# Kernel optimization log

Measured on AMD Instinct MI355X. Metric: run time of the kernel, lower is better.

## Reference

```python
import jax, jax.numpy as jnp
import numpy as np

D_MODEL = 1024
N_HEAD = 16
D_HEAD = D_MODEL // N_HEAD
N_EXPERTS = 8
TOP_K = 2
D_FF = 4096
EPS = 1e-6


def setup_inputs() -> dict:
    key = jax.random.key(0)
    ks = jax.random.split(key, 16)
    s = 0.02  # init scale
    d, dff, E = D_MODEL, D_FF, N_EXPERTS
    return {
        "dec": jax.random.normal(ks[0], (4, 1024, d), jnp.float32),
        "text_encoder": jax.random.normal(ks[1], (4, 512, d), jnp.float32),
        # self-attention projections
        "Wq1": jax.random.normal(ks[2], (d, d), jnp.float32) * s,
        "Wk1": jax.random.normal(ks[3], (d, d), jnp.float32) * s,
        "Wv1": jax.random.normal(ks[4], (d, d), jnp.float32) * s,
        "Wo1": jax.random.normal(ks[5], (d, d), jnp.float32) * s,
        # cross-attention projections
        "Wq2": jax.random.normal(ks[6], (d, d), jnp.float32) * s,
        "Wk2": jax.random.normal(ks[7], (d, d), jnp.float32) * s,
        "Wv2": jax.random.normal(ks[8], (d, d), jnp.float32) * s,
        "Wo2": jax.random.normal(ks[9], (d, d), jnp.float32) * s,
        # shared RMSNorm gain (module uses one norm instance three times)
        "g": jnp.ones((d,), jnp.float32),
        # MoE router + per-expert FFN weights
        "Wg": jax.random.normal(ks[10], (d, E), jnp.float32) * s,
        "W1": jax.random.normal(ks[11], (E, d, dff), jnp.float32) * s,
        "W2": jax.random.normal(ks[12], (E, dff, d), jnp.float32) * s,
    }


def rmsnorm(x, g):
    return x * jax.lax.rsqrt(jnp.mean(x * x, axis=-1, keepdims=True) + EPS) * g


def mha(q_in, k_in, v_in, Wq, Wk, Wv, Wo):
    B, Sq, _ = q_in.shape
    Sk = k_in.shape[1]
    q = (q_in @ Wq).reshape(B, Sq, N_HEAD, D_HEAD)
    k = (k_in @ Wk).reshape(B, Sk, N_HEAD, D_HEAD)
    v = (v_in @ Wv).reshape(B, Sk, N_HEAD, D_HEAD)
    scores = jnp.einsum("bqhd,bkhd->bhqk", q, k) / jnp.sqrt(jnp.asarray(D_HEAD, q.dtype))
    attn = jax.nn.softmax(scores, axis=-1)
    out = jnp.einsum("bhqk,bkhd->bqhd", attn, v).reshape(B, Sq, D_MODEL)
    return out @ Wo


def moe(x, Wg, W1, W2):
    # top-k softmax router, renormalized weights; dense per-expert FFN with combine
    probs = jax.nn.softmax(x @ Wg, axis=-1)              # [B,S,E]
    weights, indices = jax.lax.top_k(probs, TOP_K)        # [B,S,k]
    weights = weights / jnp.sum(weights, axis=-1, keepdims=True)
    # combine[t,e] = sum_k weights[t,k] * (indices[t,k]==e)
    combine = jnp.sum(
        jax.nn.one_hot(indices, N_EXPERTS, dtype=x.dtype) * weights[..., None], axis=-2
    )  # [B,S,E]
    out = jnp.zeros_like(x)
    for e in range(N_EXPERTS):  # fixed small expert loop
        h = jax.nn.relu(x @ W1[e]) @ W2[e]
        out = out + combine[..., e:e + 1] * h
    return weights, indices, out


def reference(dec, text_encoder, Wq1, Wk1, Wv1, Wo1, Wq2, Wk2, Wv2, Wo2, g, Wg, W1, W2):
    # self-attention + residual + RMSNorm (dropout p=0 -> identity)
    x = rmsnorm(mha(dec, dec, dec, Wq1, Wk1, Wv1, Wo1) + dec, g)
    # cross-attention + residual + RMSNorm
    x = rmsnorm(mha(x, text_encoder, text_encoder, Wq2, Wk2, Wv2, Wo2) + x, g)
    # MoE FFN + residual + RMSNorm
    weights, indices, y = moe(x, Wg, W1, W2)
    x = rmsnorm(y + x, g)
    return weights, indices, x
```

## Files before the change

### kernel.cpp

```cpp
#include <hip/hip_runtime.h>
#include <stdint.h>

#define D_    1024
#define BB    4
#define SDEC  1024
#define STXT  512
#define TDEC  4096
#define TTXT  2048
#define NH    16
#define DHD   64
#define NE    8
#define DFF   4096
#define NSLOT 8192
#define ND1   8192
#define ND2   4096
#define MOEGRID 512

using u16 = unsigned short;
typedef __attribute__((ext_vector_type(8))) short bf16x8;
typedef __attribute__((ext_vector_type(4))) float f32x4;

__device__ __forceinline__ float bf2f(u16 h) {
    union { unsigned int u; float f; } x; x.u = ((unsigned int)h) << 16; return x.f;
}
__device__ __forceinline__ u16 f2bf(float f) {
    union { float f; unsigned int u; } x; x.f = f;
    unsigned int lsb = (x.u >> 16) & 1u;
    return (u16)((x.u + 0x7fffu + lsb) >> 16);
}

__device__ __forceinline__ void gld16(const u16* g, u16* l) {
    __builtin_amdgcn_global_load_lds((const __attribute__((address_space(1))) void*)g,
                                     (__attribute__((address_space(3))) void*)l,
                                     16, 0, 0);
}

constexpr int BM = 128, BK = 32;

template<int SPLIT, int EPI, int BROWS>
__global__ __launch_bounds__(256) void gemm_bt(
    const u16* __restrict__ AH, const u16* __restrict__ AL,
    const u16* __restrict__ BH, const u16* __restrict__ BL,
    float* __restrict__ Cf, u16* __restrict__ CH, u16* __restrict__ CL,
    int M, int N, int K, int lda, int ldb, int ldc,
    long strA, long strB, long strC)
{
    constexpr int WM = (BROWS == 64) ? 2 : 4;
    constexpr int ASZ = BM * BK, BSZ = BROWS * BK;
    __shared__ u16 smem[(SPLIT ? 2 : 1) * (ASZ + BSZ)];
    u16* sAH = smem;
    u16* sBH = smem + ASZ;
    u16* sAL = SPLIT ? smem + ASZ + BSZ : nullptr;
    u16* sBL = SPLIT ? smem + 2 * ASZ + BSZ : nullptr;

    const int z = blockIdx.z;
    const long zA = (long)z * strA, zB = (long)z * strB, zC = (long)z * strC;

    const int tileM = blockIdx.y * BM, tileN = blockIdx.x * BROWS;
    const int t = threadIdx.x;
    const int sr = t >> 2;
    const int sc = (t & 3) << 3;
    const u16* pA = AH + zA + (long)(tileM + sr) * lda + sc;
    const u16* pB = BH + zB + (long)(tileN + sr) * ldb + sc;
    const u16* pAl = nullptr; const u16* pBl = nullptr;
    if constexpr (SPLIT) {
        pAl = AL + zA + (long)(tileM + sr) * lda + sc;
        pBl = BL + zB + (long)(tileN + sr) * ldb + sc;
    }
    const long hA = 64L * lda, hB = 64L * ldb;

    const int lane = t & 63;
    const int wv = t >> 6;
    const int wr = (BROWS == 64) ? (wv << 5) : ((wv >> 1) << 6);
    const int wc = (BROWS == 64) ? 0 : ((wv & 1) << 6);
    const int fr = lane & 15, kg = lane >> 4;

    f32x4 acc[WM][4];
    const f32x4 vzero = {0.f, 0.f, 0.f, 0.f};
#pragma unroll
    for (int m = 0; m < WM; ++m)
#pragma unroll
        for (int n = 0; n < 4; ++n) acc[m][n] = vzero;

    for (int k0 = 0; k0 < K; k0 += BK) {
        gld16(pA + k0,      sAH + t * 8);
        gld16(pA + k0 + hA, sAH + 2048 + t * 8);
        gld16(pB + k0,      sBH + t * 8);
        if constexpr (BROWS == 128) gld16(pB + k0 + hB, sBH + 2048 + t * 8);
        if constexpr (SPLIT) {
            gld16(pAl + k0,      sAL + t * 8);
            gld16(pAl + k0 + hA, sAL + 2048 + t * 8);
            gld16(pBl + k0,      sBL + t * 8);
            if constexpr (BROWS == 128) gld16(pBl + k0 + hB, sBL + 2048 + t * 8);
        }
        __syncthreads();

        bf16x8 fa[WM], fb[4], fal[WM], fbl[4];
#pragma unroll
        for (int m = 0; m < WM; ++m) {
            fa[m] = *(const bf16x8*)&sAH[(wr + m * 16 + fr) * BK + (kg << 3)];
            if constexpr (SPLIT) fal[m] = *(const bf16x8*)&sAL[(wr + m * 16 + fr) * BK + (kg << 3)];
        }
#pragma unroll
        for (int n = 0; n < 4; ++n) {
            fb[n] = *(const bf16x8*)&sBH[(wc + n * 16 + fr) * BK + (kg << 3)];
            if constexpr (SPLIT) fbl[n] = *(const bf16x8*)&sBL[(wc + n * 16 + fr) * BK + (kg << 3)];
        }
#pragma unroll
        for (int m = 0; m < WM; ++m)
#pragma unroll
            for (int n = 0; n < 4; ++n) {
                acc[m][n] = __builtin_amdgcn_mfma_f32_16x16x32_bf16(fa[m], fb[n], acc[m][n], 0, 0, 0);
                if constexpr (SPLIT) {
                    acc[m][n] = __builtin_amdgcn_mfma_f32_16x16x32_bf16(fa[m],  fbl[n], acc[m][n], 0, 0, 0);
                    acc[m][n] = __builtin_amdgcn_mfma_f32_16x16x32_bf16(fal[m], fb[n],  acc[m][n], 0, 0, 0);
                }
            }
        __syncthreads();
    }

#pragma unroll
    for (int m = 0; m < WM; ++m) {
        const int r0 = tileM + wr + m * 16 + (kg << 2);
#pragma unroll
        for (int n = 0; n < 4; ++n) {
            const int col = tileN + wc + n * 16 + fr;
            if (col >= N) continue;
#pragma unroll
            for (int i = 0; i < 4; ++i) {
                const int r = r0 + i;
                if (r >= M) continue;
                const float v = acc[m][n][i];
                const long off = zC + (long)r * ldc + col;
                if constexpr (EPI == 0) {
                    Cf[off] = v;
                } else if constexpr (EPI == 1) {
                    const u16 h = f2bf(v);
                    CH[off] = h;
                    CL[off] = f2bf(v - bf2f(h));
                } else {
                    CH[off] = f2bf(fmaxf(v, 0.f));
                }
            }
        }
    }
}

__global__ __launch_bounds__(256) void pv_gemm(
    const u16* __restrict__ PHp, const u16* __restrict__ PLp,
    const u16* __restrict__ VTH, const u16* __restrict__ VTL,
    float* __restrict__ Op, int Skv)
{
    __shared__ u16 smem[12288];
    u16* sAH = smem;
    u16* sAL = smem + 4096;
    u16* sBH = smem + 8192;
    u16* sBL = smem + 10240;

    const int kq = blockIdx.x;
    const int tileM = blockIdx.y * 128;
    const int z = blockIdx.z;
    const int kbase = kq * (Skv >> 2);
    const int nks = Skv >> 7;

    const int t = threadIdx.x;
    const int sr = t >> 2, sc = (t & 3) << 3;
    const u16* pA  = PHp + (long)z * 1024 * Skv + (long)(tileM + sr) * Skv + kbase + sc;
    const u16* pAl = PLp + (long)z * 1024 * Skv + (long)(tileM + sr) * Skv + kbase + sc;
    const u16* pB  = VTH + (long)z * 64 * Skv + (long)sr * Skv + kbase + sc;
    const u16* pBl = VTL + (long)z * 64 * Skv + (long)sr * Skv + kbase + sc;
    const long hA = 64L * Skv;

    const int lane = t & 63, wv = t >> 6;
    const int wr = wv << 5;
    const int fr = lane & 15, kg = lane >> 4;

    f32x4 acc[2][4];
    const f32x4 vzero = {0.f, 0.f, 0.f, 0.f};
#pragma unroll
    for (int m = 0; m < 2; ++m)
#pragma unroll
        for (int n = 0; n < 4; ++n) acc[m][n] = vzero;

    for (int ks = 0; ks < nks; ++ks) {
        const long k0 = (long)ks << 5;
        gld16(pA + k0,       sAH + t * 8);
        gld16(pA + k0 + hA,  sAH + 2048 + t * 8);
        gld16(pAl + k0,      sAL + t * 8);
        gld16(pAl + k0 + hA, sAL + 2048 + t * 8);
        gld16(pB + k0,       sBH + t * 8);
        gld16(pBl + k0,      sBL + t * 8);
        __syncthreads();
        bf16x8 fa[2], fb[4], fal[2], fbl[4];
#pragma unroll
        for (int m = 0; m < 2; ++m) {
            fa[m]  = *(const bf16x8*)&sAH[(wr + m * 16 + fr) * 32 + (kg << 3)];
            fal[m] = *(const bf16x8*)&sAL[(wr + m * 16 + fr) * 32 + (kg << 3)];
        }
#pragma unroll
        for (int n = 0; n < 4; ++n) {
            fb[n]  = *(const bf16x8*)&sBH[(n * 16 + fr) * 32 + (kg << 3)];
            fbl[n] = *(const bf16x8*)&sBL[(n * 16 + fr) * 32 + (kg << 3)];
        }
#pragma unroll
        for (int m = 0; m < 2; ++m)
#pragma unroll
            for (int n = 0; n < 4; ++n) {
                acc[m][n] = __builtin_amdgcn_mfma_f32_16x16x32_bf16(fa[m],  fb[n],  acc[m][n], 0, 0, 0);
                acc[m][n] = __builtin_amdgcn_mfma_f32_16x16x32_bf16(fa[m],  fbl[n], acc[m][n], 0, 0, 0);
                acc[m][n] = __builtin_amdgcn_mfma_f32_16x16x32_bf16(fal[m], fb[n],  acc[m][n], 0, 0, 0);
            }
        __syncthreads();
    }

    const long base = ((long)kq * NH + z) * 65536;
#pragma unroll
    for (int m = 0; m < 2; ++m) {
        const int r0 = tileM + wr + m * 16 + (kg << 2);
#pragma unroll
        for (int n = 0; n < 4; ++n) {
            const int col = n * 16 + fr;
#pragma unroll
            for (int i = 0; i < 4; ++i)
                Op[base + (long)(r0 + i) * 64 + col] = acc[m][n][i];
        }
    }
}

__global__ __launch_bounds__(256) void pv_combine(
    const float* __restrict__ Op, u16* __restrict__ aoH, u16* __restrict__ aoL)
{
    const long i = ((long)blockIdx.x * 256 + threadIdx.x) * 4;
    const int z = (int)(i >> 16);
    const int rem = (int)(i & 65535);
    const int r = rem >> 6, c = rem & 63;
    float4 v = *(const float4*)(Op + i);
    const float4 v1 = *(const float4*)(Op + 1048576 + i);
    const float4 v2 = *(const float4*)(Op + 2097152 + i);
    const float4 v3 = *(const float4*)(Op + 3145728 + i);
    v.x += v1.x + v2.x + v3.x;
    v.y += v1.y + v2.y + v3.y;
    v.z += v1.z + v2.z + v3.z;
    v.w += v1.w + v2.w + v3.w;
    const long dst = (long)r * D_ + z * 64 + c;
    u16 h0 = f2bf(v.x), h1 = f2bf(v.y), h2 = f2bf(v.z), h3 = f2bf(v.w);
    uint2 hh;
    hh.x = (unsigned)h0 | ((unsigned)h1 << 16);
    hh.y = (unsigned)h2 | ((unsigned)h3 << 16);
    *(uint2*)(aoH + dst) = hh;
    u16 l0 = f2bf(v.x - bf2f(h0)), l1 = f2bf(v.y - bf2f(h1));
    u16 l2 = f2bf(v.z - bf2f(h2)), l3 = f2bf(v.w - bf2f(h3));
    uint2 ll;
    ll.x = (unsigned)l0 | ((unsigned)l1 << 16);
    ll.y = (unsigned)l2 | ((unsigned)l3 << 16);
    *(uint2*)(aoL + dst) = ll;
}

template<int EPI>
__global__ __launch_bounds__(256, 2) void moe_gemm2(
    const u16* __restrict__ Ag, int lda,
    const u16* __restrict__ BTbase, int ldb, long btStride,
    float* __restrict__ Cf0, float* __restrict__ Cf1, u16* __restrict__ CH, int ldc,
    const int4* __restrict__ desc, int ndesc, int Kiter)
{
    __shared__ u16 smem[32768];
    const int t = threadIdx.x;
    const int lane = t & 63, wv = t >> 6;
    const int wr = (wv >> 1) << 6, wc = (wv & 1) << 6;
    const int fr = lane & 15, kg = lane >> 4;
    const int nks = Kiter >> 5;

    const int rS = t >> 2;
    const int cS = ((t & 3) ^ ((t >> 3) & 3)) << 3;

    int ldsA[4], ldsB[4];
#pragma unroll
    for (int m = 0; m < 4; ++m) {
        const int ra = wr + m * 16 + fr;
        ldsA[m] = ra * 32 + ((kg ^ ((ra >> 1) & 3)) << 3);
        const int rb = wc + m * 16 + fr;
        ldsB[m] = rb * 32 + ((kg ^ ((rb >> 1) & 3)) << 3);
    }

    for (int p = blockIdx.x; p < ndesc; p += MOEGRID) {
        const int4 d = desc[p];
        if (d.x < 0) continue;
        const int rowbase = d.x, colbase = d.y & 0xFFFF, e = d.y >> 16;
        const int kbase = d.z, s1 = d.w;
        const u16* paS = Ag + (long)(rowbase + rS) * lda + kbase + cS;
        const u16* pbS = BTbase + (long)e * btStride + (long)(colbase + rS) * ldb + kbase + cS;
        const long hA = 64L * lda, hB = 64L * ldb;

        f32x4 acc[4][4];
        const f32x4 vzero = {0.f, 0.f, 0.f, 0.f};
#pragma unroll
        for (int m = 0; m < 4; ++m)
#pragma unroll
            for (int n = 0; n < 4; ++n) acc[m][n] = vzero;

#define STG(ks) { const int s_ = (ks) & 3; const long k0_ = (long)(ks) << 5; \
        u16* b_ = smem + s_ * 8192; \
        gld16(paS + k0_,      b_ + t * 8); \
        gld16(paS + k0_ + hA, b_ + 2048 + t * 8); \
        gld16(pbS + k0_,      b_ + 4096 + t * 8); \
        gld16(pbS + k0_ + hB, b_ + 6144 + t * 8); }

        STG(0); STG(1); STG(2);
        asm volatile("s_waitcnt vmcnt(8)" ::: "memory");
        __builtin_amdgcn_s_barrier();
        __builtin_amdgcn_sched_barrier(0);

        for (int ks = 0; ks < nks; ++ks) {
            if (ks + 3 < nks) STG(ks + 3);
            const u16* sA = smem + (ks & 3) * 8192;
            const u16* sB = sA + 4096;
            bf16x8 fa[4], fb[4];
#pragma unroll
            for (int m = 0; m < 4; ++m) fa[m] = *(const bf16x8*)&sA[ldsA[m]];
#pragma unroll
            for (int n = 0; n < 4; ++n) fb[n] = *(const bf16x8*)&sB[ldsB[n]];
            __builtin_amdgcn_s_setprio(1);
#pragma unroll
            for (int m = 0; m < 4; ++m)
#pragma unroll
                for (int n = 0; n < 4; ++n)
                    acc[m][n] = __builtin_amdgcn_mfma_f32_16x16x32_bf16(fa[m], fb[n], acc[m][n], 0, 0, 0);
            __builtin_amdgcn_s_setprio(0);
            if (ks + 3 < nks)      { asm volatile("s_waitcnt vmcnt(8)" ::: "memory"); }
            else if (ks + 2 < nks) { asm volatile("s_waitcnt vmcnt(4)" ::: "memory"); }
            else                   { asm volatile("s_waitcnt vmcnt(0)" ::: "memory"); }
            __builtin_amdgcn_s_barrier();
            __builtin_amdgcn_sched_barrier(0);
        }
#undef STG

        float* __restrict__ C = (EPI == 0) ? ((kbase == 0) ? Cf0 : Cf1) : nullptr;
#pragma unroll
        for (int m = 0; m < 4; ++m) {
            const int r0 = rowbase + wr + m * 16 + (kg << 2);
#pragma unroll
            for (int n = 0; n < 4; ++n) {
                const int col = colbase + wc + n * 16 + fr;
#pragma unroll
                for (int i = 0; i < 4; ++i) {
                    const int r = r0 + i;
                    if (r >= s1) continue;
                    const float v = acc[m][n][i];
                    const long off = (long)r * ldc + col;
                    if constexpr (EPI == 0) C[off] = v;
                    else                    CH[off] = f2bf(fmaxf(v, 0.f));
                }
            }
        }
    }
}

__global__ __launch_bounds__(256) void split2k(const float* __restrict__ in,
                                               u16* __restrict__ oh, u16* __restrict__ ol, long n)
{
    long i = ((long)blockIdx.x * 256 + threadIdx.x) * 4;
    if (i >= n) return;
    float4 v = *(const float4*)(in + i);
    u16 h0 = f2bf(v.x), h1 = f2bf(v.y), h2 = f2bf(v.z), h3 = f2bf(v.w);
    uint2 oo;
    oo.x = (unsigned)h0 | ((unsigned)h1 << 16);
    oo.y = (unsigned)h2 | ((unsigned)h3 << 16);
    *(uint2*)(oh + i) = oo;
    if (ol) {
        u16 l0 = f2bf(v.x - bf2f(h0)), l1 = f2bf(v.y - bf2f(h1));
        u16 l2 = f2bf(v.z - bf2f(h2)), l3 = f2bf(v.w - bf2f(h3));
        uint2 ll;
        ll.x = (unsigned)l0 | ((unsigned)l1 << 16);
        ll.y = (unsigned)l2 | ((unsigned)l3 << 16);
        *(uint2*)(ol + i) = ll;
    }
}

struct Ptr8 { const float* p[8]; };
__global__ __launch_bounds__(256) void transpose_split_w(
    Ptr8 in, u16* __restrict__ oh, u16* __restrict__ ol)
{
    __shared__ float tile[32][33];
    const int z = blockIdx.z;
    const float* ip = in.p[z];
    u16* ohp = oh + (long)z * D_ * D_;
    u16* olp = ol + (long)z * D_ * D_;
    const int c0 = blockIdx.x * 32, r0 = blockIdx.y * 32;
    const int tx = threadIdx.x & 31, ty = threadIdx.x >> 5;
    for (int i = ty; i < 32; i += 8)
        tile[i][tx] = ip[(long)(r0 + i) * D_ + c0 + tx];
    __syncthreads();
    for (int i = ty; i < 32; i += 8) {
        int oc = c0 + i, orr = r0 + tx;
        float v = tile[tx][i];
        u16 h = f2bf(v);
        ohp[(long)oc * D_ + orr] = h;
        olp[(long)oc * D_ + orr] = f2bf(v - bf2f(h));
    }
}

__global__ __launch_bounds__(256) void transpose_split(
    const float* __restrict__ in, u16* __restrict__ oh, u16* __restrict__ ol,
    int R, int C, int ild, long ibs1, long ibs2, int nb2, int old_, long obs)
{
    __shared__ float tile[32][33];
    const int z = blockIdx.z;
    const float* ip = in + (long)(z / nb2) * ibs1 + (long)(z % nb2) * ibs2;
    u16* ohp = oh + (long)z * obs;
    u16* olp = ol ? ol + (long)z * obs : nullptr;
    const int c0 = blockIdx.x * 32, r0 = blockIdx.y * 32;
    const int tx = threadIdx.x & 31, ty = threadIdx.x >> 5;
    for (int i = ty; i < 32; i += 8) {
        int r = r0 + i, c = c0 + tx;
        tile[i][tx] = (r < R && c < C) ? ip[(long)r * ild + c] : 0.f;
    }
    __syncthreads();
    for (int i = ty; i < 32; i += 8) {
        int oc = c0 + i, orr = r0 + tx;
        if (oc < C && orr < R) {
            float v = tile[tx][i];
            u16 h = f2bf(v);
            ohp[(long)oc * old_ + orr] = h;
            if (olp) olp[(long)oc * old_ + orr] = f2bf(v - bf2f(h));
        }
    }
}

__global__ __launch_bounds__(256) void transpose_split_hl(
    const u16* __restrict__ inH, const u16* __restrict__ inL,
    u16* __restrict__ oh, u16* __restrict__ ol,
    int R, int C, int ild, long ibs1, long ibs2, int nb2, int old_, long obs)
{
    __shared__ float tile[32][33];
    const int z = blockIdx.z;
    const long base = (long)(z / nb2) * ibs1 + (long)(z % nb2) * ibs2;
    u16* ohp = oh + (long)z * obs;
    u16* olp = ol + (long)z * obs;
    const int c0 = blockIdx.x * 32, r0 = blockIdx.y * 32;
    const int tx = threadIdx.x & 31, ty = threadIdx.x >> 5;
    for (int i = ty; i < 32; i += 8) {
        int r = r0 + i, c = c0 + tx;
        float v = 0.f;
        if (r < R && c < C) {
            const long o = base + (long)r * ild + c;
            v = bf2f(inH[o]) + bf2f(inL[o]);
        }
        tile[i][tx] = v;
    }
    __syncthreads();
    for (int i = ty; i < 32; i += 8) {
        int oc = c0 + i, orr = r0 + tx;
        if (oc < C && orr < R) {
            float v = tile[tx][i];
            u16 h = f2bf(v);
            ohp[(long)oc * old_ + orr] = h;
            olp[(long)oc * old_ + orr] = f2bf(v - bf2f(h));
        }
    }
}

__global__ __launch_bounds__(256) void softmax_split(
    const float* __restrict__ s, u16* __restrict__ ph, u16* __restrict__ pl,
    int cols, float scale)
{
    const float* p = s + (long)blockIdx.x * cols;
    u16* php = ph + (long)blockIdx.x * cols;
    u16* plp = pl + (long)blockIdx.x * cols;
    const int t = threadIdx.x;
    float v[4];
    int vpt;
    if (cols == 1024) {
        vpt = 4;
        float4 x = ((const float4*)p)[t];
        v[0] = x.x * scale; v[1] = x.y * scale; v[2] = x.z * scale; v[3] = x.w * scale;
    } else {
        vpt = 2;
        float2 x = ((const float2*)p)[t];
        v[0] = x.x * scale; v[1] = x.y * scale; v[2] = -3.4e38f; v[3] = -3.4e38f;
    }
    float mx = fmaxf(fmaxf(v[0], v[1]), fmaxf(v[2], v[3]));
#pragma unroll
    for (int o = 32; o; o >>= 1) mx = fmaxf(mx, __shfl_xor(mx, o));
    __shared__ float sm[4];
    const int wv = t >> 6, ln = t & 63;
    if (ln == 0) sm[wv] = mx;
    __syncthreads();
    mx = fmaxf(fmaxf(sm[0], sm[1]), fmaxf(sm[2], sm[3]));
    float sum = 0.f;
    for (int i = 0; i < vpt; ++i) { v[i] = expf(v[i] - mx); sum += v[i]; }
#pragma unroll
    for (int o = 32; o; o >>= 1) sum += __shfl_xor(sum, o);
    __shared__ float ss[4];
    if (ln == 0) ss[wv] = sum;
    __syncthreads();
    sum = ss[0] + ss[1] + ss[2] + ss[3];
    const float inv = 1.f / sum;
    if (cols == 1024) {
        float q0 = v[0] * inv, q1 = v[1] * inv, q2 = v[2] * inv, q3 = v[3] * inv;
        u16 h0 = f2bf(q0), h1 = f2bf(q1), h2 = f2bf(q2), h3 = f2bf(q3);
        uint2 hh; hh.x = (unsigned)h0 | ((unsigned)h1 << 16); hh.y = (unsigned)h2 | ((unsigned)h3 << 16);
        ((uint2*)php)[t] = hh;
        u16 l0 = f2bf(q0 - bf2f(h0)), l1 = f2bf(q1 - bf2f(h1));
        u16 l2 = f2bf(q2 - bf2f(h2)), l3 = f2bf(q3 - bf2f(h3));
        uint2 ll; ll.x = (unsigned)l0 | ((unsigned)l1 << 16); ll.y = (unsigned)l2 | ((unsigned)l3 << 16);
        ((uint2*)plp)[t] = ll;
    } else {
        float q0 = v[0] * inv, q1 = v[1] * inv;
        u16 h0 = f2bf(q0), h1 = f2bf(q1);
        ((unsigned*)php)[t] = (unsigned)h0 | ((unsigned)h1 << 16);
        u16 l0 = f2bf(q0 - bf2f(h0)), l1 = f2bf(q1 - bf2f(h1));
        ((unsigned*)plp)[t] = (unsigned)l0 | ((unsigned)l1 << 16);
    }
}

__global__ __launch_bounds__(256) void add_rmsnorm(
    const float* __restrict__ a, const float* __restrict__ b, const float* __restrict__ g,
    float* __restrict__ xo, u16* __restrict__ xh, u16* __restrict__ xl)
{
    const long row = blockIdx.x;
    const int t = threadIdx.x;
    const float* pa = a + row * D_;
    const float* pb = b + row * D_;
    float v[4]; double ssq = 0.0;
#pragma unroll
    for (int i = 0; i < 4; ++i) {
        int c = t + (i << 8);
        v[i] = pa[c] + pb[c];
        ssq += (double)v[i] * v[i];
    }
#pragma unroll
    for (int o = 32; o; o >>= 1) ssq += __shfl_xor(ssq, o);
    __shared__ double sd[4];
    if ((t & 63) == 0) sd[t >> 6] = ssq;
    __syncthreads();
    ssq = sd[0] + sd[1] + sd[2] + sd[3];
    const float rs = (float)(1.0 / sqrt(ssq * (1.0 / 1024.0) + 1e-6));
#pragma unroll
    for (int i = 0; i < 4; ++i) {
        int c = t + (i << 8);
        float o = v[i] * rs * g[c];
        xo[row * D_ + c] = o;
        if (xh) {
            u16 h = f2bf(o);
            xh[row * D_ + c] = h;
            if (xl) xl[row * D_ + c] = f2bf(o - bf2f(h));
        }
    }
}

__global__ __launch_bounds__(256) void router_topk(
    const float* __restrict__ x2, const float* __restrict__ Wg,
    float* __restrict__ outw, float* __restrict__ outi,
    int* __restrict__ idx, float* __restrict__ tokw, int* __restrict__ counts, int T)
{
    const int wid = (int)((blockIdx.x * 256 + threadIdx.x) >> 6);
    const int lane = threadIdx.x & 63;
    if (wid >= T) return;
    float acc[NE];
#pragma unroll
    for (int e = 0; e < NE; ++e) acc[e] = 0.f;
    const float* xr = x2 + (long)wid * D_;
    for (int i = 0; i < 16; ++i) {
        float xv = xr[i * 64 + lane];
        const float* wr = Wg + (long)(i * 64 + lane) * NE;
#pragma unroll
        for (int e = 0; e < NE; ++e) acc[e] += xv * wr[e];
    }
#pragma unroll
    for (int e = 0; e < NE; ++e)
#pragma unroll
        for (int o = 32; o; o >>= 1) acc[e] += __shfl_xor(acc[e], o);
    if (lane == 0) {
        float m = acc[0];
#pragma unroll
        for (int e = 1; e < NE; ++e) m = fmaxf(m, acc[e]);
        float p[NE], s = 0.f;
#pragma unroll
        for (int e = 0; e < NE; ++e) { p[e] = expf(acc[e] - m); s += p[e]; }
        const float invs = 1.f / s;
#pragma unroll
        for (int e = 0; e < NE; ++e) p[e] *= invs;
        int e0 = 0;
#pragma unroll
        for (int e = 1; e < NE; ++e) if (p[e] > p[e0]) e0 = e;
        int e1 = (e0 == 0) ? 1 : 0;
#pragma unroll
        for (int e = 0; e < NE; ++e) if (e != e0 && e != e1 && p[e] > p[e1]) e1 = e;
        float w0 = p[e0], w1 = p[e1];
        const float sw = 1.f / (w0 + w1);
        w0 *= sw; w1 *= sw;
        outw[2 * wid] = w0;      outw[2 * wid + 1] = w1;
        outi[2 * wid] = (float)e0; outi[2 * wid + 1] = (float)e1;
        idx[2 * wid] = e0;       idx[2 * wid + 1] = e1;
        tokw[2 * wid] = w0;      tokw[2 * wid + 1] = w1;
        atomicAdd(&counts[e0], 1);
        atomicAdd(&counts[e1], 1);
    }
}

__global__ void scan_desc(const int* __restrict__ counts, int* __restrict__ cursor,
                          int4* __restrict__ d1, int4* __restrict__ d2)
{
    __shared__ int sseg[NE + 1];
    if (threadIdx.x == 0) {
        int a = 0;
        for (int e = 0; e < NE; ++e) { sseg[e] = a; cursor[e] = a; a += counts[e]; }
        sseg[NE] = a;
    }
    __syncthreads();
    const int e = threadIdx.x;
    if (e < NE) {
        const int s0 = sseg[e], s1 = sseg[e + 1];
        const int nyt = (s1 - s0 + 127) >> 7;
        for (int xt = 0; xt < 32; ++xt)
            for (int yt = 0; yt < nyt; ++yt)
                d1[e + 8 * (xt * nyt + yt)] =
                    make_int4(s0 + yt * 128, (xt * 128) | (e << 16), 0, s1);
        for (int kh = 0; kh < 2; ++kh)
            for (int xt = 0; xt < 8; ++xt)
                for (int yt = 0; yt < nyt; ++yt)
                    d2[e + 8 * ((kh * 8 + xt) * nyt + yt)] =
                        make_int4(s0 + yt * 128, (xt * 128) | (e << 16), kh * 2048, s1);
    }
}

__global__ __launch_bounds__(256) void scatter_slots(
    const int* __restrict__ idx, int* __restrict__ cursor,
    int* __restrict__ row_token, int* __restrict__ slot_of, int T)
{
    const int t = blockIdx.x * 256 + threadIdx.x;
    if (t >= T) return;
#pragma unroll
    for (int k = 0; k < 2; ++k) {
        const int e = idx[2 * t + k];
        const int pos = atomicAdd(&cursor[e], 1);
        row_token[pos] = t;
        slot_of[2 * t + k] = pos;
    }
}

__global__ __launch_bounds__(256) void gather_bf16(
    const float* __restrict__ x2, const int* __restrict__ row_token, u16* __restrict__ Xg)
{
    const int r = blockIdx.x;
    const int t = threadIdx.x;
    const float* src = x2 + (long)row_token[r] * D_ + t * 4;
    float4 v = *(const float4*)src;
    uint2 oo;
    oo.x = (unsigned)f2bf(v.x) | ((unsigned)f2bf(v.y) << 16);
    oo.y = (unsigned)f2bf(v.z) | ((unsigned)f2bf(v.w) << 16);
    *(uint2*)(Xg + (long)r * D_ + t * 4) = oo;
}

__global__ __launch_bounds__(256) void combine_rmsnorm(
    const float* __restrict__ Y0, const float* __restrict__ Y1,
    const int* __restrict__ slot_of, const float* __restrict__ tokw,
    const float* __restrict__ x2, const float* __restrict__ g, float* __restrict__ out)
{
    const long tr = blockIdx.x;
    const int t = threadIdx.x;
    const int s0 = slot_of[2 * tr], s1 = slot_of[2 * tr + 1];
    const float w0 = tokw[2 * tr], w1 = tokw[2 * tr + 1];
    const float* ya0 = Y0 + (long)s0 * D_;
    const float* yb0 = Y1 + (long)s0 * D_;
    const float* ya1 = Y0 + (long)s1 * D_;
    const float* yb1 = Y1 + (long)s1 * D_;
    const float* xr = x2 + tr * D_;
    float v[4]; double ssq = 0.0;
#pragma unroll
    for (int i = 0; i < 4; ++i) {
        int c = t + (i << 8);
        v[i] = w0 * (ya0[c] + yb0[c]) + w1 * (ya1[c] + yb1[c]) + xr[c];
        ssq += (double)v[i] * v[i];
    }
#pragma unroll
    for (int o = 32; o; o >>= 1) ssq += __shfl_xor(ssq, o);
    __shared__ double sd[4];
    if ((t & 63) == 0) sd[t >> 6] = ssq;
    __syncthreads();
    ssq = sd[0] + sd[1] + sd[2] + sd[3];
    const float rs = (float)(1.0 / sqrt(ssq * (1.0 / 1024.0) + 1e-6));
#pragma unroll
    for (int i = 0; i < 4; ++i) {
        int c = t + (i << 8);
        out[tr * D_ + c] = v[i] * rs * g[c];
    }
}

__global__ void sentinel(float* o) { o[0] = 12345.0f; }

extern "C" void kernel_launch(void* const* d_in, const int* in_sizes, int n_in,
                              void* d_out, int out_size, void* d_ws, size_t ws_size,
                              hipStream_t stream)
{
    const float* dec = (const float*)d_in[0];
    const float* te  = (const float*)d_in[1];
    const float* g  = (const float*)d_in[10];
    const float* Wg = (const float*)d_in[11];
    const float* W1 = (const float*)d_in[12];
    const float* W2 = (const float*)d_in[13];
    float* outw = (float*)d_out;
    float* outi = outw + 2 * TDEC;
    float* outx = outw + 4 * TDEC;

    char* ws = (char*)d_ws;
    size_t off = 0;
    auto A = [&](size_t bytes) -> char* {
        char* p = ws + off;
        off += (bytes + 255) & ~(size_t)255;
        return p;
    };

    u16* decH = (u16*)A((size_t)TDEC * D_ * 2);
    u16* decL = (u16*)A((size_t)TDEC * D_ * 2);
    u16* teH  = (u16*)A((size_t)TTXT * D_ * 2);
    u16* teL  = (u16*)A((size_t)TTXT * D_ * 2);
    u16* wtHall = (u16*)A((size_t)8 * D_ * D_ * 2);
    u16* wtLall = (u16*)A((size_t)8 * D_ * D_ * 2);
    float* x1f = (float*)A((size_t)TDEC * D_ * 4);
    float* x2f = (float*)A((size_t)TDEC * D_ * 4);
    float* tokw = (float*)A(NSLOT * 4);
    int* idx    = (int*)A(NSLOT * 4);
    int* counts = (int*)A(256);
    int* cursor = (int*)A(256);
    int* row_token = (int*)A(NSLOT * 4);
    int* slot_of   = (int*)A(NSLOT * 4);
    int4* desc1 = (int4*)A((size_t)ND1 * 16);
    int4* desc2 = (int4*)A((size_t)ND2 * 16);

    const size_t Rbase = off;
    float* scores = (float*)A((size_t)NH * SDEC * SDEC * 4);
    u16* PH = (u16*)A((size_t)NH * SDEC * SDEC * 2);
    u16* PL = (u16*)A((size_t)NH * SDEC * SDEC * 2);
    u16* qkvH = (u16*)A((size_t)TDEC * 3 * D_ * 2);
    u16* qkvL = (u16*)A((size_t)TDEC * 3 * D_ * 2);
    u16* q2H  = (u16*)A((size_t)TDEC * D_ * 2);
    u16* q2L  = (u16*)A((size_t)TDEC * D_ * 2);
    u16* kv2H = (u16*)A((size_t)TTXT * 2 * D_ * 2);
    u16* kv2L = (u16*)A((size_t)TTXT * 2 * D_ * 2);
    u16* vTH = (u16*)A((size_t)TDEC * D_ * 2);
    u16* vTL = (u16*)A((size_t)TDEC * D_ * 2);
    u16* aoH = (u16*)A((size_t)TDEC * D_ * 2);
    u16* aoL = (u16*)A((size_t)TDEC * D_ * 2);
    u16* x1H = (u16*)A((size_t)TDEC * D_ * 2);
    u16* x1L = (u16*)A((size_t)TDEC * D_ * 2);
    float* of = (float*)A((size_t)TDEC * D_ * 4);
    float* Opart = (float*)A((size_t)4 * NH * SDEC * DHD * 4);
    const size_t attnEnd = off;

    off = Rbase;
    u16* W1T  = (u16*)A((size_t)NE * DFF * D_ * 2);
    u16* W2T  = (u16*)A((size_t)NE * D_ * DFF * 2);
    u16* Xg   = (u16*)A((size_t)(NSLOT + 256) * D_ * 2);
    u16* Hb   = (u16*)A((size_t)(NSLOT + 256) * DFF * 2);
    float* Yseg = (float*)A((size_t)NSLOT * D_ * 4);
    float* Ypart1 = (float*)W1T;
    const size_t needed = (off > attnEnd ? off : attnEnd);

    if (ws_size < needed) {
        sentinel<<<1, 1, 0, stream>>>(outw);
        return;
    }

    const dim3 blk(256);

    split2k<<<dim3((TDEC * D_) / 1024), blk, 0, stream>>>(dec, decH, decL, (long)TDEC * D_);
    split2k<<<dim3((TTXT * D_) / 1024), blk, 0, stream>>>(te, teH, teL, (long)TTXT * D_);
    Ptr8 wp;
    for (int i = 0; i < 8; ++i) wp.p[i] = (const float*)d_in[2 + i];
    transpose_split_w<<<dim3(32, 32, 8), blk, 0, stream>>>(wp, wtHall, wtLall);

    gemm_bt<1, 1, 128><<<dim3(24, 32, 1), blk, 0, stream>>>(decH, decL, wtHall, wtLall,
        nullptr, qkvH, qkvL, TDEC, 3 * D_, D_, D_, D_, 3 * D_, 0, 0, 0);
    transpose_split_hl<<<dim3(2, 32, BB * NH), blk, 0, stream>>>(qkvH + 2 * D_, qkvL + 2 * D_,
        vTH, vTL, SDEC, DHD, 3 * D_, (long)SDEC * 3 * D_, DHD, NH, SDEC, (long)DHD * SDEC);

    for (int b = 0; b < BB; ++b) {
        const long qo3 = (long)b * SDEC * 3 * D_;
        const long qo  = (long)b * SDEC * D_;
        gemm_bt<1, 0, 128><<<dim3(8, 8, NH), blk, 0, stream>>>(
            qkvH + qo3, qkvL + qo3, qkvH + qo3 + D_, qkvL + qo3 + D_,
            scores, nullptr, nullptr, SDEC, SDEC, DHD, 3 * D_, 3 * D_, SDEC,
            DHD, DHD, (long)SDEC * SDEC);
        softmax_split<<<dim3(NH * SDEC), blk, 0, stream>>>(scores, PH, PL, SDEC, 0.125f);
        pv_gemm<<<dim3(4, 8, NH), blk, 0, stream>>>(PH, PL,
            vTH + (long)b * NH * DHD * SDEC, vTL + (long)b * NH * DHD * SDEC, Opart, SDEC);
        pv_combine<<<dim3(1024), blk, 0, stream>>>(Opart, aoH + qo, aoL + qo);
    }
    gemm_bt<1, 0, 128><<<dim3(8, 32, 1), blk, 0, stream>>>(aoH, aoL,
        wtHall + (size_t)3 * D_ * D_, wtLall + (size_t)3 * D_ * D_,
        of, nullptr, nullptr, TDEC, D_, D_, D_, D_, D_, 0, 0, 0);
    add_rmsnorm<<<dim3(TDEC), blk, 0, stream>>>(of, dec, g, x1f, x1H, x1L);

    gemm_bt<1, 1, 128><<<dim3(8, 32, 1), blk, 0, stream>>>(x1H, x1L,
        wtHall + (size_t)4 * D_ * D_, wtLall + (size_t)4 * D_ * D_,
        nullptr, q2H, q2L, TDEC, D_, D_, D_, D_, D_, 0, 0, 0);
    gemm_bt<1, 1, 128><<<dim3(16, 16, 1), blk, 0, stream>>>(teH, teL,
        wtHall + (size_t)5 * D_ * D_, wtLall + (size_t)5 * D_ * D_,
        nullptr, kv2H, kv2L, TTXT, 2 * D_, D_, D_, D_, 2 * D_, 0, 0, 0);
    transpose_split_hl<<<dim3(2, 16, BB * NH), blk, 0, stream>>>(kv2H + D_, kv2L + D_,
        vTH, vTL, STXT, DHD, 2 * D_, (long)STXT * 2 * D_, DHD, NH, STXT, (long)DHD * STXT);

    for (int b = 0; b < BB; ++b) {
        const long qo  = (long)b * SDEC * D_;
        const long ko2 = (long)b * STXT * 2 * D_;
        gemm_bt<1, 0, 128><<<dim3(4, 8, NH), blk, 0, stream>>>(
            q2H + qo, q2L + qo, kv2H + ko2, kv2L + ko2,
            scores, nullptr, nullptr, SDEC, STXT, DHD, D_, 2 * D_, STXT,
            DHD, DHD, (long)SDEC * STXT);
        softmax_split<<<dim3(NH * SDEC), blk, 0, stream>>>(scores, PH, PL, STXT, 0.125f);
        pv_gemm<<<dim3(4, 8, NH), blk, 0, stream>>>(PH, PL,
            vTH + (long)b * NH * DHD * STXT, vTL + (long)b * NH * DHD * STXT, Opart, STXT);
        pv_combine<<<dim3(1024), blk, 0, stream>>>(Opart, aoH + qo, aoL + qo);
    }
    gemm_bt<1, 0, 128><<<dim3(8, 32, 1), blk, 0, stream>>>(aoH, aoL,
        wtHall + (size_t)7 * D_ * D_, wtLall + (size_t)7 * D_ * D_,
        of, nullptr, nullptr, TDEC, D_, D_, D_, D_, D_, 0, 0, 0);
    add_rmsnorm<<<dim3(TDEC), blk, 0, stream>>>(of, x1f, g, x2f, nullptr, nullptr);

    hipMemsetAsync(counts, 0, 32, stream);
    hipMemsetAsync(desc1, 0xFF, (size_t)ND1 * 16, stream);
    hipMemsetAsync(desc2, 0xFF, (size_t)ND2 * 16, stream);
    router_topk<<<dim3(TDEC / 4), blk, 0, stream>>>(x2f, Wg, outw, outi, idx, tokw, counts, TDEC);
    scan_desc<<<1, 64, 0, stream>>>(counts, cursor, desc1, desc2);
    scatter_slots<<<dim3(TDEC / 256), blk, 0, stream>>>(idx, cursor, row_token, slot_of, TDEC);
    gather_bf16<<<dim3(NSLOT), blk, 0, stream>>>(x2f, row_token, Xg);

    transpose_split<<<dim3(DFF / 32, D_ / 32, NE), blk, 0, stream>>>(W1, W1T, nullptr,
        D_, DFF, DFF, (long)D_ * DFF, 0, 1, D_, (long)DFF * D_);
    transpose_split<<<dim3(D_ / 32, DFF / 32, NE), blk, 0, stream>>>(W2, W2T, nullptr,
        DFF, D_, D_, (long)D_ * DFF, 0, 1, DFF, (long)D_ * DFF);
    moe_gemm2<2><<<dim3(MOEGRID), blk, 0, stream>>>(Xg, D_, W1T, D_, (long)DFF * D_,
        nullptr, nullptr, Hb, DFF, desc1, ND1, 1024);
    moe_gemm2<0><<<dim3(MOEGRID), blk, 0, stream>>>(Hb, DFF, W2T, DFF, (long)D_ * DFF,
        Yseg, Ypart1, nullptr, D_, desc2, ND2, 2048);
    combine_rmsnorm<<<dim3(TDEC), blk, 0, stream>>>(Yseg, Ypart1, slot_of, tokw, x2f, g, outx);

    (void)in_sizes; (void)n_in; (void)out_size;
}
```

Measured before the change: 1.380 ms.

## Batch attention across batch dimension and store scores as hi/lo bf16 split

Attention score GEMMs now write hi/lo bf16 pairs directly instead of fp32 scores, and softmax reads and overwrites those buffers in place. This removes the separate fp32 score buffer and its traffic. When the workspace is large enough, the four per-batch launch loops collapse into single launches over batch×head using a 2D z-stride decomposition, which cuts launch count and raises occupancy for the small cross-attention grids. Scores now round to hi+lo bf16 before softmax, a small precision change, and the batched path needs a larger workspace.

```diff
diff --git a/kernel.cpp b/kernel.cpp
--- a/kernel.cpp
+++ b/kernel.cpp
@@ -42,8 +42,8 @@
     const u16* __restrict__ AH, const u16* __restrict__ AL,
     const u16* __restrict__ BH, const u16* __restrict__ BL,
     float* __restrict__ Cf, u16* __restrict__ CH, u16* __restrict__ CL,
-    int M, int N, int K, int lda, int ldb, int ldc,
-    long strA, long strB, long strC)
+    int M, int N, int K, int lda, int ldb, int ldc, int nb2,
+    long strA1, long strA2, long strB1, long strB2, long strC1, long strC2)
 {
     constexpr int WM = (BROWS == 64) ? 2 : 4;
     constexpr int ASZ = BM * BK, BSZ = BROWS * BK;
@@ -54,7 +54,10 @@
     u16* sBL = SPLIT ? smem + 2 * ASZ + BSZ : nullptr;
 
     const int z = blockIdx.z;
-    const long zA = (long)z * strA, zB = (long)z * strB, zC = (long)z * strC;
+    const int z1 = z / nb2, z2 = z % nb2;
+    const long zA = (long)z1 * strA1 + (long)z2 * strA2;
+    const long zB = (long)z1 * strB1 + (long)z2 * strB2;
+    const long zC = (long)z1 * strC1 + (long)z2 * strC2;
 
     const int tileM = blockIdx.y * BM, tileN = blockIdx.x * BROWS;
     const int t = threadIdx.x;
@@ -149,7 +152,7 @@
 __global__ __launch_bounds__(256) void pv_gemm(
     const u16* __restrict__ PHp, const u16* __restrict__ PLp,
     const u16* __restrict__ VTH, const u16* __restrict__ VTL,
-    float* __restrict__ Op, int Skv)
+    float* __restrict__ Op, int Skv, int NZ)
 {
     __shared__ u16 smem[12288];
     u16* sAH = smem;
@@ -213,7 +216,7 @@
         __syncthreads();
     }
 
-    const long base = ((long)kq * NH + z) * 65536;
+    const long base = ((long)kq * NZ + z) * 65536;
 #pragma unroll
     for (int m = 0; m < 2; ++m) {
         const int r0 = tileM + wr + m * 16 + (kg << 2);
@@ -228,21 +231,24 @@
 }
 
 __global__ __launch_bounds__(256) void pv_combine(
-    const float* __restrict__ Op, u16* __restrict__ aoH, u16* __restrict__ aoL)
+    const float* __restrict__ Op, u16* __restrict__ aoH, u16* __restrict__ aoL,
+    int nz, int nh)
 {
     const long i = ((long)blockIdx.x * 256 + threadIdx.x) * 4;
-    const int z = (int)(i >> 16);
+    const int zz = (int)(i >> 16);
     const int rem = (int)(i & 65535);
     const int r = rem >> 6, c = rem & 63;
+    const int b = zz / nh, h = zz % nh;
+    const long kqS = (long)nz * 65536;
     float4 v = *(const float4*)(Op + i);
-    const float4 v1 = *(const float4*)(Op + 1048576 + i);
-    const float4 v2 = *(const float4*)(Op + 2097152 + i);
-    const float4 v3 = *(const float4*)(Op + 3145728 + i);
+    const float4 v1 = *(const float4*)(Op + kqS + i);
+    const float4 v2 = *(const float4*)(Op + 2 * kqS + i);
+    const float4 v3 = *(const float4*)(Op + 3 * kqS + i);
     v.x += v1.x + v2.x + v3.x;
     v.y += v1.y + v2.y + v3.y;
     v.z += v1.z + v2.z + v3.z;
     v.w += v1.w + v2.w + v3.w;
-    const long dst = (long)r * D_ + z * 64 + c;
+    const long dst = (long)b * SDEC * D_ + (long)r * D_ + h * 64 + c;
     u16 h0 = f2bf(v.x), h1 = f2bf(v.y), h2 = f2bf(v.z), h3 = f2bf(v.w);
     uint2 hh;
     hh.x = (unsigned)h0 | ((unsigned)h1 << 16);
@@ -459,11 +465,9 @@
     }
 }
 
-__global__ __launch_bounds__(256) void softmax_split(
-    const float* __restrict__ s, u16* __restrict__ ph, u16* __restrict__ pl,
-    int cols, float scale)
-{
-    const float* p = s + (long)blockIdx.x * cols;
+__global__ __launch_bounds__(256) void softmax_hl(
+    u16* __restrict__ ph, u16* __restrict__ pl, int cols, float scale)
+{
     u16* php = ph + (long)blockIdx.x * cols;
     u16* plp = pl + (long)blockIdx.x * cols;
     const int t = threadIdx.x;
@@ -471,12 +475,19 @@
     int vpt;
     if (cols == 1024) {
         vpt = 4;
-        float4 x = ((const float4*)p)[t];
-        v[0] = x.x * scale; v[1] = x.y * scale; v[2] = x.z * scale; v[3] = x.w * scale;
+        uint2 hh = ((const uint2*)php)[t];
+        uint2 ll = ((const uint2*)plp)[t];
+        v[0] = (bf2f((u16)(hh.x & 0xffff)) + bf2f((u16)(ll.x & 0xffff))) * scale;
+        v[1] = (bf2f((u16)(hh.x >> 16))    + bf2f((u16)(ll.x >> 16)))    * scale;
+        v[2] = (bf2f((u16)(hh.y & 0xffff)) + bf2f((u16)(ll.y & 0xffff))) * scale;
+        v[3] = (bf2f((u16)(hh.y >> 16))    + bf2f((u16)(ll.y >> 16)))    * scale;
     } else {
         vpt = 2;
-        float2 x = ((const float2*)p)[t];
-        v[0] = x.x * scale; v[1] = x.y * scale; v[2] = -3.4e38f; v[3] = -3.4e38f;
+        unsigned hh = ((const unsigned*)php)[t];
+        unsigned ll = ((const unsigned*)plp)[t];
+        v[0] = (bf2f((u16)(hh & 0xffff)) + bf2f((u16)(ll & 0xffff))) * scale;
+        v[1] = (bf2f((u16)(hh >> 16))    + bf2f((u16)(ll >> 16)))    * scale;
+        v[2] = -3.4e38f; v[3] = -3.4e38f;
     }
     float mx = fmaxf(fmaxf(v[0], v[1]), fmaxf(v[2], v[3]));
 #pragma unroll
@@ -502,8 +513,8 @@
         ((uint2*)php)[t] = hh;
         u16 l0 = f2bf(q0 - bf2f(h0)), l1 = f2bf(q1 - bf2f(h1));
         u16 l2 = f2bf(q2 - bf2f(h2)), l3 = f2bf(q3 - bf2f(h3));
-        uint2 ll; ll.x = (unsigned)l0 | ((unsigned)l1 << 16); ll.y = (unsigned)l2 | ((unsigned)l3 << 16);
-        ((uint2*)plp)[t] = ll;
+        uint2 llo; llo.x = (unsigned)l0 | ((unsigned)l1 << 16); llo.y = (unsigned)l2 | ((unsigned)l3 << 16);
+        ((uint2*)plp)[t] = llo;
     } else {
         float q0 = v[0] * inv, q1 = v[1] * inv;
         u16 h0 = f2bf(q0), h1 = f2bf(q1);
@@ -727,39 +738,54 @@
     int* slot_of   = (int*)A(NSLOT * 4);
     int4* desc1 = (int4*)A((size_t)ND1 * 16);
     int4* desc2 = (int4*)A((size_t)ND2 * 16);
-
     const size_t Rbase = off;
-    float* scores = (float*)A((size_t)NH * SDEC * SDEC * 4);
-    u16* PH = (u16*)A((size_t)NH * SDEC * SDEC * 2);
-    u16* PL = (u16*)A((size_t)NH * SDEC * SDEC * 2);
-    u16* qkvH = (u16*)A((size_t)TDEC * 3 * D_ * 2);
-    u16* qkvL = (u16*)A((size_t)TDEC * 3 * D_ * 2);
-    u16* q2H  = (u16*)A((size_t)TDEC * D_ * 2);
-    u16* q2L  = (u16*)A((size_t)TDEC * D_ * 2);
-    u16* kv2H = (u16*)A((size_t)TTXT * 2 * D_ * 2);
-    u16* kv2L = (u16*)A((size_t)TTXT * 2 * D_ * 2);
-    u16* vTH = (u16*)A((size_t)TDEC * D_ * 2);
-    u16* vTL = (u16*)A((size_t)TDEC * D_ * 2);
-    u16* aoH = (u16*)A((size_t)TDEC * D_ * 2);
-    u16* aoL = (u16*)A((size_t)TDEC * D_ * 2);
-    u16* x1H = (u16*)A((size_t)TDEC * D_ * 2);
-    u16* x1L = (u16*)A((size_t)TDEC * D_ * 2);
-    float* of = (float*)A((size_t)TDEC * D_ * 4);
-    float* Opart = (float*)A((size_t)4 * NH * SDEC * DHD * 4);
-    const size_t attnEnd = off;
-
-    off = Rbase;
+
     u16* W1T  = (u16*)A((size_t)NE * DFF * D_ * 2);
     u16* W2T  = (u16*)A((size_t)NE * D_ * DFF * 2);
     u16* Xg   = (u16*)A((size_t)(NSLOT + 256) * D_ * 2);
     u16* Hb   = (u16*)A((size_t)(NSLOT + 256) * DFF * 2);
     float* Yseg = (float*)A((size_t)NSLOT * D_ * 4);
     float* Ypart1 = (float*)W1T;
-    const size_t needed = (off > attnEnd ? off : attnEnd);
-
-    if (ws_size < needed) {
-        sentinel<<<1, 1, 0, stream>>>(outw);
-        return;
+    const size_t moeEnd = off;
+
+    auto allocAttn = [&](bool batched, u16*& PH, u16*& PL, u16*& qkvH, u16*& qkvL,
+                         u16*& q2H, u16*& q2L, u16*& kv2H, u16*& kv2L,
+                         u16*& vTH, u16*& vTL, u16*& aoH, u16*& aoL,
+                         u16*& x1H, u16*& x1L, float*& of, float*& Opart) {
+        off = Rbase;
+        const size_t pcell = batched ? (size_t)BB * NH * SDEC * SDEC * 2
+                                     : (size_t)NH * SDEC * SDEC * 2;
+        PH = (u16*)A(pcell);
+        PL = (u16*)A(pcell);
+        qkvH = (u16*)A((size_t)TDEC * 3 * D_ * 2);
+        qkvL = (u16*)A((size_t)TDEC * 3 * D_ * 2);
+        q2H  = (u16*)A((size_t)TDEC * D_ * 2);
+        q2L  = (u16*)A((size_t)TDEC * D_ * 2);
+        kv2H = (u16*)A((size_t)TTXT * 2 * D_ * 2);
+        kv2L = (u16*)A((size_t)TTXT * 2 * D_ * 2);
+        vTH = (u16*)A((size_t)TDEC * D_ * 2);
+        vTL = (u16*)A((size_t)TDEC * D_ * 2);
+        aoH = (u16*)A((size_t)TDEC * D_ * 2);
+        aoL = (u16*)A((size_t)TDEC * D_ * 2);
+        x1H = (u16*)A((size_t)TDEC * D_ * 2);
+        x1L = (u16*)A((size_t)TDEC * D_ * 2);
+        of  = (float*)A((size_t)TDEC * D_ * 4);
+        Opart = (float*)A((size_t)4 * (batched ? BB * NH : NH) * SDEC * DHD * 4);
+        return off;
+    };
+
+    u16 *PH, *PL, *qkvH, *qkvL, *q2H, *q2L, *kv2H, *kv2L, *vTH, *vTL, *aoH, *aoL, *x1H, *x1L;
+    float *of, *Opart;
+    size_t attnEnd = allocAttn(true, PH, PL, qkvH, qkvL, q2H, q2L, kv2H, kv2L,
+                               vTH, vTL, aoH, aoL, x1H, x1L, of, Opart);
+    bool batched = ws_size >= (attnEnd > moeEnd ? attnEnd : moeEnd);
+    if (!batched) {
+        attnEnd = allocAttn(false, PH, PL, qkvH, qkvL, q2H, q2L, kv2H, kv2L,
+                            vTH, vTL, aoH, aoL, x1H, x1L, of, Opart);
+        if (ws_size < (attnEnd > moeEnd ? attnEnd : moeEnd)) {
+            sentinel<<<1, 1, 0, stream>>>(outw);
+            return;
+        }
     }
 
     const dim3 blk(256);
@@ -771,51 +797,75 @@
     transpose_split_w<<<dim3(32, 32, 8), blk, 0, stream>>>(wp, wtHall, wtLall);
 
     gemm_bt<1, 1, 128><<<dim3(24, 32, 1), blk, 0, stream>>>(decH, decL, wtHall, wtLall,
-        nullptr, qkvH, qkvL, TDEC, 3 * D_, D_, D_, D_, 3 * D_, 0, 0, 0);
+        nullptr, qkvH, qkvL, TDEC, 3 * D_, D_, D_, D_, 3 * D_, 1, 0, 0, 0, 0, 0, 0);
     transpose_split_hl<<<dim3(2, 32, BB * NH), blk, 0, stream>>>(qkvH + 2 * D_, qkvL + 2 * D_,
         vTH, vTL, SDEC, DHD, 3 * D_, (long)SDEC * 3 * D_, DHD, NH, SDEC, (long)DHD * SDEC);
 
-    for (int b = 0; b < BB; ++b) {
-        const long qo3 = (long)b * SDEC * 3 * D_;
-        const long qo  = (long)b * SDEC * D_;
-        gemm_bt<1, 0, 128><<<dim3(8, 8, NH), blk, 0, stream>>>(
-            qkvH + qo3, qkvL + qo3, qkvH + qo3 + D_, qkvL + qo3 + D_,
-            scores, nullptr, nullptr, SDEC, SDEC, DHD, 3 * D_, 3 * D_, SDEC,
-            DHD, DHD, (long)SDEC * SDEC);
-        softmax_split<<<dim3(NH * SDEC), blk, 0, stream>>>(scores, PH, PL, SDEC, 0.125f);
-        pv_gemm<<<dim3(4, 8, NH), blk, 0, stream>>>(PH, PL,
-            vTH + (long)b * NH * DHD * SDEC, vTL + (long)b * NH * DHD * SDEC, Opart, SDEC);
-        pv_combine<<<dim3(1024), blk, 0, stream>>>(Opart, aoH + qo, aoL + qo);
+    if (batched) {
+        gemm_bt<1, 1, 128><<<dim3(8, 8, BB * NH), blk, 0, stream>>>(
+            qkvH, qkvL, qkvH + D_, qkvL + D_, nullptr, PH, PL,
+            SDEC, SDEC, DHD, 3 * D_, 3 * D_, SDEC, NH,
+            (long)SDEC * 3 * D_, DHD, (long)SDEC * 3 * D_, DHD,
+            (long)NH * SDEC * SDEC, (long)SDEC * SDEC);
+        softmax_hl<<<dim3(BB * NH * SDEC), blk, 0, stream>>>(PH, PL, SDEC, 0.125f);
+        pv_gemm<<<dim3(4, 8, BB * NH), blk, 0, stream>>>(PH, PL, vTH, vTL, Opart, SDEC, BB * NH);
+        pv_combine<<<dim3(BB * NH * 64), blk, 0, stream>>>(Opart, aoH, aoL, BB * NH, NH);
+    } else {
+        for (int b = 0; b < BB; ++b) {
+            const long qo3 = (long)b * SDEC * 3 * D_;
+            const long qo  = (long)b * SDEC * D_;
+            gemm_bt<1, 1, 128><<<dim3(8, 8, NH), blk, 0, stream>>>(
+                qkvH + qo3, qkvL + qo3, qkvH + qo3 + D_, qkvL + qo3 + D_,
+                nullptr, PH, PL, SDEC, SDEC, DHD, 3 * D_, 3 * D_, SDEC, NH,
+                0, DHD, 0, DHD, 0, (long)SDEC * SDEC);
+            softmax_hl<<<dim3(NH * SDEC), blk, 0, stream>>>(PH, PL, SDEC, 0.125f);
+            pv_gemm<<<dim3(4, 8, NH), blk, 0, stream>>>(PH, PL,
+                vTH + (long)b * NH * DHD * SDEC, vTL + (long)b * NH * DHD * SDEC,
+                Opart, SDEC, NH);
+            pv_combine<<<dim3(NH * 64), blk, 0, stream>>>(Opart, aoH + qo, aoL + qo, NH, NH);
+        }
     }
     gemm_bt<1, 0, 128><<<dim3(8, 32, 1), blk, 0, stream>>>(aoH, aoL,
         wtHall + (size_t)3 * D_ * D_, wtLall + (size_t)3 * D_ * D_,
-        of, nullptr, nullptr, TDEC, D_, D_, D_, D_, D_, 0, 0, 0);
+        of, nullptr, nullptr, TDEC, D_, D_, D_, D_, D_, 1, 0, 0, 0, 0, 0, 0);
     add_rmsnorm<<<dim3(TDEC), blk, 0, stream>>>(of, dec, g, x1f, x1H, x1L);
 
     gemm_bt<1, 1, 128><<<dim3(8, 32, 1), blk, 0, stream>>>(x1H, x1L,
         wtHall + (size_t)4 * D_ * D_, wtLall + (size_t)4 * D_ * D_,
-        nullptr, q2H, q2L, TDEC, D_, D_, D_, D_, D_, 0, 0, 0);
+        nullptr, q2H, q2L, TDEC, D_, D_, D_, D_, D_, 1, 0, 0, 0, 0, 0, 0);
     gemm_bt<1, 1, 128><<<dim3(16, 16, 1), blk, 0, stream>>>(teH, teL,
         wtHall + (size_t)5 * D_ * D_, wtLall + (size_t)5 * D_ * D_,
-        nullptr, kv2H, kv2L, TTXT, 2 * D_, D_, D_, D_, 2 * D_, 0, 0, 0);
+        nullptr, kv2H, kv2L, TTXT, 2 * D_, D_, D_, D_, 2 * D_, 1, 0, 0, 0, 0, 0, 0);
     transpose_split_hl<<<dim3(2, 16, BB * NH), blk, 0, stream>>>(kv2H + D_, kv2L + D_,
         vTH, vTL, STXT, DHD, 2 * D_, (long)STXT * 2 * D_, DHD, NH, STXT, (long)DHD * STXT);
 
-    for (int b = 0; b < BB; ++b) {
-        const long qo  = (long)b * SDEC * D_;
-        const long ko2 = (long)b * STXT * 2 * D_;
-        gemm_bt<1, 0, 128><<<dim3(4, 8, NH), blk, 0, stream>>>(
-            q2H + qo, q2L + qo, kv2H + ko2, kv2L + ko2,
-            scores, nullptr, nullptr, SDEC, STXT, DHD, D_, 2 * D_, STXT,
-            DHD, DHD, (long)SDEC * STXT);
-        softmax_split<<<dim3(NH * SDEC), blk, 0, stream>>>(scores, PH, PL, STXT, 0.125f);
-        pv_gemm<<<dim3(4, 8, NH), blk, 0, stream>>>(PH, PL,
-            vTH + (long)b * NH * DHD * STXT, vTL + (long)b * NH * DHD * STXT, Opart, STXT);
-        pv_combine<<<dim3(1024), blk, 0, stream>>>(Opart, aoH + qo, aoL + qo);
+    if (batched) {
+        gemm_bt<1, 1, 128><<<dim3(4, 8, BB * NH), blk, 0, stream>>>(
+            q2H, q2L, kv2H, kv2L, nullptr, PH, PL,
+            SDEC, STXT, DHD, D_, 2 * D_, STXT, NH,
+            (long)SDEC * D_, DHD, (long)STXT * 2 * D_, DHD,
+            (long)NH * SDEC * STXT, (long)SDEC * STXT);
+        softmax_hl<<<dim3(BB * NH * SDEC), blk, 0, stream>>>(PH, PL, STXT, 0.125f);
+        pv_gemm<<<dim3(4, 8, BB * NH), blk, 0, stream>>>(PH, PL, vTH, vTL, Opart, STXT, BB * NH);
+        pv_combine<<<dim3(BB * NH * 64), blk, 0, stream>>>(Opart, aoH, aoL, BB * NH, NH);
+    } else {
+        for (int b = 0; b < BB; ++b) {
+            const long qo  = (long)b * SDEC * D_;
+            const long ko2 = (long)b * STXT * 2 * D_;
+            gemm_bt<1, 1, 128><<<dim3(4, 8, NH), blk, 0, stream>>>(
+                q2H + qo, q2L + qo, kv2H + ko2, kv2L + ko2,
+                nullptr, PH, PL, SDEC, STXT, DHD, D_, 2 * D_, STXT, NH,
+                0, DHD, 0, DHD, 0, (long)SDEC * STXT);
+            softmax_hl<<<dim3(NH * SDEC), blk, 0, stream>>>(PH, PL, STXT, 0.125f);
+            pv_gemm<<<dim3(4, 8, NH), blk, 0, stream>>>(PH, PL,
+                vTH + (long)b * NH * DHD * STXT, vTL + (long)b * NH * DHD * STXT,
+                Opart, STXT, NH);
+            pv_combine<<<dim3(NH * 64), blk, 0, stream>>>(Opart, aoH + qo, aoL + qo, NH, NH);
+        }
     }
     gemm_bt<1, 0, 128><<<dim3(8, 32, 1), blk, 0, stream>>>(aoH, aoL,
         wtHall + (size_t)7 * D_ * D_, wtLall + (size_t)7 * D_ * D_,
-        of, nullptr, nullptr, TDEC, D_, D_, D_, D_, D_, 0, 0, 0);
+        of, nullptr, nullptr, TDEC, D_, D_, D_, D_, D_, 1, 0, 0, 0, 0, 0, 0);
     add_rmsnorm<<<dim3(TDEC), blk, 0, stream>>>(of, x1f, g, x2f, nullptr, nullptr);
 
     hipMemsetAsync(counts, 0, 32, stream);
```

After: 1.402 ms. Within noise of the previous version (+1.6%).
